# Kernel tuning notes

Hardware: AMD Instinct MI355X
Metric: run time of the kernel (lower is better)

The kernel has to match this reference:

```python
import jax, jax.numpy as jnp
import numpy as np

B, T, D, H, O = 64, 1000, 16, 1024, 8
DT, TAU, G, PROB_CONN = 0.1, 1.0, 1.5, 0.25


def setup_inputs() -> dict:
    key = jax.random.key(0)
    k_in, k_h0, k_i2h, k_mask, k_val, k_h2o = jax.random.split(key, 6)
    inp = jax.random.normal(k_in, (B, T, D), dtype=jnp.float32)
    hidden = jax.random.normal(k_h0, (B, H), dtype=jnp.float32)
    # i2h: 1/sqrt(D) * randn(H, D)
    W_i2h = jax.random.normal(k_i2h, (H, D), dtype=jnp.float32) / np.sqrt(D)
    # h2h: sparse Gaussian, connection prob PROB_CONN, no self-connections,
    # std = g / sqrt(prob_conn * H)
    mask = (jax.random.uniform(k_mask, (H, H)) < PROB_CONN).astype(jnp.float32)
    mask = mask * (1.0 - jnp.eye(H, dtype=jnp.float32))
    sigma = G / np.sqrt(PROB_CONN * H)
    W_h2h = jax.random.normal(k_val, (H, H), dtype=jnp.float32) * sigma * mask
    # h2o: 1/sqrt(H) * randn(O, H)
    W_h2o = jax.random.normal(k_h2o, (O, H), dtype=jnp.float32) / np.sqrt(H)
    return {"input": inp, "hidden": hidden, "W_i2h": W_i2h, "W_h2h": W_h2h, "W_h2o": W_h2o}


def reference(input, hidden, W_i2h, W_h2h, W_h2o):
    a = DT / TAU  # leak factor
    # precompute input projection for all timesteps: [B,T,H]
    x_proj = jnp.einsum('btd,hd->bth', input, W_i2h)
    xs = jnp.swapaxes(x_proj, 0, 1)  # [T,B,H]

    def step(h, x_t):
        h = (1.0 - a) * h + a * (jnp.tanh(h) @ W_h2h.T + x_t)
        out = jnp.tanh(h) @ W_h2o.T
        return h, (out, h)

    _, (outs, hs) = jax.lax.scan(step, hidden, xs)
    outputs = jnp.swapaxes(outs, 0, 1)  # [B,T,O]
    hiddens = jnp.swapaxes(hs, 0, 1)    # [B,T,H]
    return outputs, hiddens
```

## Files before the change

kernel.cpp:

```cpp
#include <hip/hip_runtime.h>
#include <hip/hip_bf16.h>

#define BB 64
#define TT 1000
#define DD 16
#define HH 1024
#define OO 8

#define NGRP 16
#define GB   4
#define SJ   64
#define NJS  16
#define NBLK 256
#define NTH  512

__global__ __launch_bounds__(NTH, 1) void rnn_coop(
    const float* __restrict__ x,
    const float* __restrict__ h0,
    const float* __restrict__ Wi2h,
    const float* Wh2h,
    float* __restrict__ out_h,
    float* TH,
    unsigned* flags)
{
    __shared__ __align__(16) float THl[8][4][GB][36];
    __shared__ float SC[2][GB][SJ][9];
    __shared__ float XS[2][GB][20];

    const int tid = threadIdx.x;
    const int w   = tid >> 6;
    const int l   = tid & 63;
    const int bid = blockIdx.x;
    const int bg  = bid & (NGRP - 1);
    const int js  = bid >> 4;

    const int j16 = l & 15;
    const int k4  = l >> 4;
    const int jbase = js * SJ + j16 * 4;
    const int kbase = w * 128 + k4 * 32;

    float4 w4[4][8];
#pragma unroll
    for (int jj = 0; jj < 4; ++jj) {
        const float* a = &Wh2h[(size_t)(jbase + jj) * HH + kbase];
        asm volatile(
            "global_load_dwordx4 %0, %8, off\n\t"
            "global_load_dwordx4 %1, %8, off offset:16\n\t"
            "global_load_dwordx4 %2, %8, off offset:32\n\t"
            "global_load_dwordx4 %3, %8, off offset:48\n\t"
            "global_load_dwordx4 %4, %8, off offset:64\n\t"
            "global_load_dwordx4 %5, %8, off offset:80\n\t"
            "global_load_dwordx4 %6, %8, off offset:96\n\t"
            "global_load_dwordx4 %7, %8, off offset:112\n\t"
            "s_waitcnt vmcnt(0)"
            : "=&v"(w4[jj][0]), "=&v"(w4[jj][1]), "=&v"(w4[jj][2]), "=&v"(w4[jj][3]),
              "=&v"(w4[jj][4]), "=&v"(w4[jj][5]), "=&v"(w4[jj][6]), "=&v"(w4[jj][7])
            : "v"(a));
    }

    const int fb = tid >> 6, fj = tid & 63;
    float h = 0.f;
    float wi[DD];
    if (tid < 256) {
        h = h0[(size_t)(bg * GB + fb) * HH + js * SJ + fj];
#pragma unroll
        for (int d = 0; d < DD; ++d) wi[d] = Wi2h[(js * SJ + fj) * DD + d];
        float th0 = tanhf(h);
        __hip_atomic_store(&TH[((size_t)(0 * NGRP + bg) * GB + fb) * HH + js * SJ + fj],
                           th0, __ATOMIC_RELAXED, __HIP_MEMORY_SCOPE_AGENT);
        asm volatile("s_waitcnt vmcnt(0)" ::: "memory");
        if (l == 0)
            __hip_atomic_store(&flags[((size_t)(0 * NGRP + bg) * NJS + js) * 16 + fb],
                               1u, __ATOMIC_RELAXED, __HIP_MEMORY_SCOPE_AGENT);
    }

    for (int t = 0; t < TT; ++t) {
        const int p = t & 1;

        {
            const unsigned target = (unsigned)(t + 1);
            const unsigned* fa = flags +
                ((size_t)(p * NGRP + bg) * NJS + (2 * w + (l >> 2))) * 16 + (l & 3);
            for (;;) {
                unsigned v = target;
                if (l < 8)
                    v = __hip_atomic_load(fa, __ATOMIC_RELAXED, __HIP_MEMORY_SCOPE_AGENT);
                if (__all((int)(v >= target))) break;
                __builtin_amdgcn_s_sleep(1);
            }
        }

        {
            const int sb = l >> 4, sq = l & 15;
            const float* base = TH + ((size_t)(p * NGRP + bg) * GB + sb) * HH + w * 128;
            const float* a0 = base + sq * 4;
            const float* a1 = base + (sq + 16) * 4;
            float4 v0, v1;
            asm volatile("global_load_dwordx4 %0, %2, off sc0 sc1\n\t"
                         "global_load_dwordx4 %1, %3, off sc0 sc1\n\t"
                         "s_waitcnt vmcnt(0)"
                         : "=&v"(v0), "=&v"(v1)
                         : "v"(a0), "v"(a1)
                         : "memory");
            int k40 = sq >> 3,        kk0 = (sq & 7) ^ k40;
            int k41 = (sq + 16) >> 3, kk1 = (sq & 7) ^ k41;
            *(float4*)&THl[w][k40][sb][kk0 * 4] = v0;
            *(float4*)&THl[w][k41][sb][kk1 * 4] = v1;
        }
        if (w == 0 && l < 16) {
            int sb2 = l >> 2, dq = (l & 3) * 4;
            float4 v = *(const float4*)&x[((size_t)(bg * GB + sb2) * TT + t) * DD + dq];
            *(float4*)&XS[p][sb2][dq] = v;
        }
        asm volatile("s_waitcnt lgkmcnt(0)" ::: "memory");
        __builtin_amdgcn_sched_barrier(0);

        float acc[4][4];
#pragma unroll
        for (int jj = 0; jj < 4; ++jj)
#pragma unroll
            for (int m = 0; m < 4; ++m) acc[jj][m] = 0.f;
#pragma unroll
        for (int kq = 0; kq < 8; ++kq) {
            const int kks = (kq ^ k4) * 4;
#pragma unroll
            for (int m = 0; m < 4; ++m) {
                float4 tv = *(const float4*)&THl[w][k4][m][kks];
#pragma unroll
                for (int jj = 0; jj < 4; ++jj) {
                    acc[jj][m] += w4[jj][kq].x * tv.x;
                    acc[jj][m] += w4[jj][kq].y * tv.y;
                    acc[jj][m] += w4[jj][kq].z * tv.z;
                    acc[jj][m] += w4[jj][kq].w * tv.w;
                }
            }
        }

#pragma unroll
        for (int jj = 0; jj < 4; ++jj)
#pragma unroll
            for (int m = 0; m < 4; ++m) {
                float a = acc[jj][m];
                a += __shfl_xor(a, 16, 64);
                a += __shfl_xor(a, 32, 64);
                acc[jj][m] = a;
            }
        if (k4 == 0) {
#pragma unroll
            for (int m = 0; m < 4; ++m)
#pragma unroll
                for (int jj = 0; jj < 4; ++jj)
                    SC[p][m][j16 * 4 + jj][w] = acc[jj][m];
        }

        __syncthreads();

        if (tid < 256) {
            float z = 0.f;
#pragma unroll
            for (int ww = 0; ww < 8; ++ww) z += SC[p][fb][fj][ww];
            float xp = 0.f;
#pragma unroll
            for (int d = 0; d < DD; ++d) xp += wi[d] * XS[p][fb][d];
            h = 0.9f * h + 0.1f * (z + xp);
            float th = tanhf(h);
            __hip_atomic_store(
                &TH[((size_t)((p ^ 1) * NGRP + bg) * GB + fb) * HH + js * SJ + fj],
                th, __ATOMIC_RELAXED, __HIP_MEMORY_SCOPE_AGENT);
            asm volatile("s_waitcnt vmcnt(0)" ::: "memory");
            if (l == 0 && t + 1 < TT)
                __hip_atomic_store(
                    &flags[((size_t)((p ^ 1) * NGRP + bg) * NJS + js) * 16 + fb],
                    (unsigned)(t + 2), __ATOMIC_RELAXED, __HIP_MEMORY_SCOPE_AGENT);
            out_h[((size_t)(bg * GB + fb) * TT + t) * HH + js * SJ + fj] = h;
        }
    }
}

__global__ __launch_bounds__(256) void h2o_kernel(
    const float* __restrict__ hs, const float* __restrict__ Wh2o,
    float* __restrict__ out_o)
{
    __shared__ float Wl[OO * HH];
    for (int i = threadIdx.x; i < OO * HH; i += 256) Wl[i] = Wh2o[i];
    __syncthreads();

    const int w = threadIdx.x >> 6, l = threadIdx.x & 63;
    const size_t nrows = (size_t)BB * TT;
    for (size_t row = (size_t)blockIdx.x * 4 + w; row < nrows; row += (size_t)gridDim.x * 4) {
        const float* hr = hs + row * HH;
        float po[OO] = {0.f};
#pragma unroll
        for (int i = 0; i < 16; ++i) {
            int j = l + 64 * i;
            float th = tanhf(hr[j]);
#pragma unroll
            for (int o = 0; o < OO; ++o) po[o] += th * Wl[o * HH + j];
        }
#pragma unroll
        for (int s = 32; s; s >>= 1)
#pragma unroll
            for (int o = 0; o < OO; ++o) po[o] += __shfl_down(po[o], s, 64);
        if (l == 0) {
#pragma unroll
            for (int o = 0; o < OO; ++o) out_o[row * OO + o] = po[o];
        }
    }
}

__global__ __launch_bounds__(512) void rnn_fallback(
    const float* __restrict__ x, const float* __restrict__ h0,
    const float* __restrict__ Wi2h, const float* __restrict__ W,
    const float* __restrict__ Wh2o, float* __restrict__ out_o,
    float* __restrict__ out_h)
{
    const int b = blockIdx.x, t0 = threadIdx.x, j0 = 2 * t0;
    const int wave = t0 >> 6, lane = t0 & 63;
    __shared__ float th[HH];
    __shared__ float xs[DD];
    __shared__ float ored[8][OO];
    float wi[2][DD];
#pragma unroll
    for (int d = 0; d < DD; ++d) {
        wi[0][d] = Wi2h[j0 * DD + d];
        wi[1][d] = Wi2h[(j0 + 1) * DD + d];
    }
    float wo[2][OO];
#pragma unroll
    for (int o = 0; o < OO; ++o) {
        wo[0][o] = Wh2o[o * HH + j0];
        wo[1][o] = Wh2o[o * HH + j0 + 1];
    }
    float h[2] = { h0[b * HH + j0], h0[b * HH + j0 + 1] };
    th[j0] = tanhf(h[0]); th[j0 + 1] = tanhf(h[1]);
    if (t0 < DD) xs[t0] = x[(size_t)(b * TT) * DD + t0];
    __syncthreads();
    for (int t = 0; t < TT; ++t) {
        float a0 = 0.f, a1 = 0.f;
        const float* r0 = W + (size_t)j0 * HH;
        const float* r1 = W + (size_t)(j0 + 1) * HH;
#pragma unroll 4
        for (int k = 0; k < HH; k += 4) {
            float4 t4 = *(const float4*)&th[k];
            float4 wA = *(const float4*)(r0 + k);
            float4 wB = *(const float4*)(r1 + k);
            a0 += t4.x * wA.x + t4.y * wA.y + t4.z * wA.z + t4.w * wA.w;
            a1 += t4.x * wB.x + t4.y * wB.y + t4.z * wB.z + t4.w * wB.w;
        }
        float xp0 = 0.f, xp1 = 0.f;
#pragma unroll
        for (int d = 0; d < DD; ++d) { xp0 += xs[d] * wi[0][d]; xp1 += xs[d] * wi[1][d]; }
        h[0] = 0.9f * h[0] + 0.1f * (a0 + xp0);
        h[1] = 0.9f * h[1] + 0.1f * (a1 + xp1);
        float th0 = tanhf(h[0]), th1 = tanhf(h[1]);
        *(float2*)&out_h[((size_t)b * TT + t) * HH + j0] = make_float2(h[0], h[1]);
        float po[OO];
#pragma unroll
        for (int o = 0; o < OO; ++o) po[o] = th0 * wo[0][o] + th1 * wo[1][o];
#pragma unroll
        for (int s = 32; s; s >>= 1)
#pragma unroll
            for (int o = 0; o < OO; ++o) po[o] += __shfl_down(po[o], s, 64);
        __syncthreads();
        if (lane == 0)
#pragma unroll
            for (int o = 0; o < OO; ++o) ored[wave][o] = po[o];
        th[j0] = th0; th[j0 + 1] = th1;
        if (t0 < DD && t + 1 < TT) xs[t0] = x[(size_t)(b * TT + t + 1) * DD + t0];
        __syncthreads();
        if (t0 < OO) {
            float s = 0.f;
#pragma unroll
            for (int ww = 0; ww < 8; ++ww) s += ored[ww][t0];
            out_o[((size_t)b * TT + t) * OO + t0] = s;
        }
    }
}

extern "C" void kernel_launch(void* const* d_in, const int* in_sizes, int n_in,
                              void* d_out, int out_size, void* d_ws, size_t ws_size,
                              hipStream_t stream) {
    const float* x    = (const float*)d_in[0];
    const float* h0   = (const float*)d_in[1];
    const float* Wi2h = (const float*)d_in[2];
    const float* Wh2h = (const float*)d_in[3];
    const float* Wh2o = (const float*)d_in[4];

    float* out_o = (float*)d_out;
    float* out_h = out_o + (size_t)BB * TT * OO;

    const size_t th_bytes   = (size_t)2 * NGRP * GB * HH * sizeof(float);
    const size_t flag_bytes = (size_t)2 * NGRP * NJS * 16 * sizeof(unsigned);

    if (ws_size >= th_bytes + flag_bytes) {
        float*    TH  = (float*)d_ws;
        unsigned* flg = (unsigned*)((char*)d_ws + th_bytes);
        hipMemsetAsync(flg, 0, flag_bytes, stream);
        rnn_coop<<<NBLK, NTH, 0, stream>>>(x, h0, Wi2h, Wh2h, out_h, TH, flg);
        h2o_kernel<<<2048, 256, 0, stream>>>(out_h, Wh2o, out_o);
    } else {
        rnn_fallback<<<BB, 512, 0, stream>>>(x, h0, Wi2h, Wh2h, Wh2o, out_o, out_h);
    }
}
```

Baseline: 5.007 ms.

## Split recurrent work into 512 blocks of 32 columns and precompute input projection

Adds a rnn_sj32 kernel that partitions each batch group's hidden columns into 32-wide slices, so 512 blocks of 512 threads each hold half as many h2h weights in registers. Its launch bounds allow several blocks per CU, which spreads the per-step matvec and reduction over more CUs. Separately, a new xproj_kernel precomputes the input projection for all timesteps into workspace, so each step loads one value instead of doing a 16-term dot product. In exchange, each step's barrier now involves twice as many producer blocks, and the spin-wait polls twice as many flags. The old 256-block kernel is kept as a fallback, and the path taken depends on workspace size and the occupancy query.

```diff
diff --git a/kernel.cpp b/kernel.cpp
--- a/kernel.cpp
+++ b/kernel.cpp
@@ -9,23 +9,53 @@
 
 #define NGRP 16
 #define GB   4
-#define SJ   64
-#define NJS  16
-#define NBLK 256
 #define NTH  512
 
-__global__ __launch_bounds__(NTH, 1) void rnn_coop(
+typedef unsigned long long u64;
+
+__global__ __launch_bounds__(256) void xproj_kernel(
+    const float* __restrict__ x,
+    const float* __restrict__ Wi2h,
+    float* __restrict__ xp)
+{
+    __shared__ float Wl[1024 * 17];
+    for (int i = threadIdx.x; i < 1024 * 16; i += 256)
+        Wl[(i >> 4) * 17 + (i & 15)] = Wi2h[i];
+    __syncthreads();
+
+    const int nrows = BB * TT;
+    for (int row = blockIdx.x; row < nrows; row += gridDim.x) {
+        float4 xa = *(const float4*)&x[(size_t)row * 16];
+        float4 xb = *(const float4*)&x[(size_t)row * 16 + 4];
+        float4 xc = *(const float4*)&x[(size_t)row * 16 + 8];
+        float4 xd = *(const float4*)&x[(size_t)row * 16 + 12];
+#pragma unroll
+        for (int c = 0; c < 4; ++c) {
+            int hh = threadIdx.x + 256 * c;
+            const float* wr = &Wl[hh * 17];
+            float s = xa.x * wr[0]  + xa.y * wr[1]  + xa.z * wr[2]  + xa.w * wr[3]
+                    + xb.x * wr[4]  + xb.y * wr[5]  + xb.z * wr[6]  + xb.w * wr[7]
+                    + xc.x * wr[8]  + xc.y * wr[9]  + xc.z * wr[10] + xc.w * wr[11]
+                    + xd.x * wr[12] + xd.y * wr[13] + xd.z * wr[14] + xd.w * wr[15];
+            xp[(size_t)row * HH + hh] = s;
+        }
+    }
+}
+
+template <int XPRE>
+__global__ __launch_bounds__(NTH, 4) void rnn_sj32(
     const float* __restrict__ x,
     const float* __restrict__ h0,
     const float* __restrict__ Wi2h,
     const float* Wh2h,
+    const float* __restrict__ xp,
     float* __restrict__ out_h,
     float* TH,
     unsigned* flags)
 {
-    __shared__ __align__(16) float THl[8][4][GB][36];
-    __shared__ float SC[2][GB][SJ][9];
-    __shared__ float XS[2][GB][20];
+    __shared__ __align__(16) float THl[8][4][164];
+    __shared__ float SC[2][4][32][9];
+    __shared__ float XS[2][4][20];
 
     const int tid = threadIdx.x;
     const int w   = tid >> 6;
@@ -34,9 +64,170 @@
     const int bg  = bid & (NGRP - 1);
     const int js  = bid >> 4;
 
+    const int j8 = l & 7;
+    const int k8 = l >> 3;
+    const int jbase = js * 32 + j8 * 4;
+    const int kbase = w * 128 + k8 * 16;
+
+    float4 w4[4][4];
+#pragma unroll
+    for (int jj = 0; jj < 4; ++jj) {
+        const float* a = &Wh2h[(size_t)(jbase + jj) * HH + kbase];
+        asm volatile(
+            "global_load_dwordx4 %0, %4, off\n\t"
+            "global_load_dwordx4 %1, %4, off offset:16\n\t"
+            "global_load_dwordx4 %2, %4, off offset:32\n\t"
+            "global_load_dwordx4 %3, %4, off offset:48\n\t"
+            "s_waitcnt vmcnt(0)"
+            : "=&v"(w4[jj][0]), "=&v"(w4[jj][1]), "=&v"(w4[jj][2]), "=&v"(w4[jj][3])
+            : "v"(a));
+    }
+
+    const int fj = tid & 31, fb = (tid >> 5) & 3;
+    float h = 0.f;
+    float wi[DD];
+    if (tid < 128) {
+        h = h0[(size_t)(bg * GB + fb) * HH + js * 32 + fj];
+        if (!XPRE) {
+#pragma unroll
+            for (int d = 0; d < DD; ++d) wi[d] = Wi2h[(js * 32 + fj) * DD + d];
+        }
+        float th0 = tanhf(h);
+        __hip_atomic_store(&TH[((size_t)(0 * NGRP + bg) * GB + fb) * HH + js * 32 + fj],
+                           th0, __ATOMIC_RELAXED, __HIP_MEMORY_SCOPE_AGENT);
+        asm volatile("s_waitcnt vmcnt(0)" ::: "memory");
+        if ((tid & 63) == 0)
+            __hip_atomic_store(
+                &flags[((size_t)(0 * NGRP + bg) * 32 + js) * 16 + (tid >> 6)],
+                1u, __ATOMIC_RELAXED, __HIP_MEMORY_SCOPE_AGENT);
+    }
+
+    for (int t = 0; t < TT; ++t) {
+        const int p = t & 1;
+
+        float xpv = 0.f;
+        if (XPRE && tid < 128)
+            xpv = xp[((size_t)(bg * GB + fb) * TT + t) * HH + js * 32 + fj];
+
+        {
+            const unsigned target = (unsigned)(t + 1);
+            const unsigned* fa = flags +
+                ((size_t)(p * NGRP + bg) * 32 + (4 * w + (l >> 1))) * 16 + (l & 1);
+            for (;;) {
+                unsigned v = target;
+                if (l < 8)
+                    v = __hip_atomic_load(fa, __ATOMIC_RELAXED, __HIP_MEMORY_SCOPE_AGENT);
+                if (__all((int)(v >= target))) break;
+                __builtin_amdgcn_s_sleep(1);
+            }
+        }
+
+        {
+            const int b = l & 3, Q0 = l >> 2;
+            const float* base = TH + ((size_t)(p * NGRP + bg) * GB + b) * HH + w * 128;
+            const float* a0 = base + Q0 * 4;
+            const float* a1 = base + (Q0 + 16) * 4;
+            float4 v0, v1;
+            asm volatile("global_load_dwordx4 %0, %2, off sc0 sc1\n\t"
+                         "global_load_dwordx4 %1, %3, off sc0 sc1\n\t"
+                         "s_waitcnt vmcnt(0)"
+                         : "=&v"(v0), "=&v"(v1)
+                         : "v"(a0), "v"(a1)
+                         : "memory");
+            *(float4*)&THl[w][b][(Q0 >> 2) * 20 + (Q0 & 3) * 4] = v0;
+            *(float4*)&THl[w][b][((Q0 + 16) >> 2) * 20 + (Q0 & 3) * 4] = v1;
+        }
+        if (!XPRE && w == 0 && l < 16) {
+            int sb2 = l >> 2, dq = (l & 3) * 4;
+            float4 v = *(const float4*)&x[((size_t)(bg * GB + sb2) * TT + t) * DD + dq];
+            *(float4*)&XS[p][sb2][dq] = v;
+        }
+        asm volatile("s_waitcnt lgkmcnt(0)" ::: "memory");
+        __builtin_amdgcn_sched_barrier(0);
+
+        float acc[4][4];
+#pragma unroll
+        for (int jj = 0; jj < 4; ++jj)
+#pragma unroll
+            for (int m = 0; m < 4; ++m) acc[jj][m] = 0.f;
+#pragma unroll
+        for (int kq = 0; kq < 4; ++kq) {
+#pragma unroll
+            for (int m = 0; m < 4; ++m) {
+                float4 tv = *(const float4*)&THl[w][m][k8 * 20 + kq * 4];
+#pragma unroll
+                for (int jj = 0; jj < 4; ++jj) {
+                    acc[jj][m] += w4[jj][kq].x * tv.x;
+                    acc[jj][m] += w4[jj][kq].y * tv.y;
+                    acc[jj][m] += w4[jj][kq].z * tv.z;
+                    acc[jj][m] += w4[jj][kq].w * tv.w;
+                }
+            }
+        }
+
+#pragma unroll
+        for (int jj = 0; jj < 4; ++jj)
+#pragma unroll
+            for (int m = 0; m < 4; ++m) {
+                float a = acc[jj][m];
+                a += __shfl_xor(a, 8, 64);
+                a += __shfl_xor(a, 16, 64);
+                a += __shfl_xor(a, 32, 64);
+                acc[jj][m] = a;
+            }
+        if (l < 8) {
+#pragma unroll
+            for (int m = 0; m < 4; ++m)
+#pragma unroll
+                for (int jj = 0; jj < 4; ++jj)
+                    SC[p][m][l * 4 + jj][w] = acc[jj][m];
+        }
+
+        __syncthreads();
+
+        if (tid < 128) {
+            float z = 0.f;
+#pragma unroll
+            for (int ww = 0; ww < 8; ++ww) z += SC[p][fb][fj][ww];
+            if (!XPRE) {
+                xpv = 0.f;
+#pragma unroll
+                for (int d = 0; d < DD; ++d) xpv += wi[d] * XS[p][fb][d];
+            }
+            h = 0.9f * h + 0.1f * (z + xpv);
+            float th = tanhf(h);
+            __hip_atomic_store(
+                &TH[((size_t)((p ^ 1) * NGRP + bg) * GB + fb) * HH + js * 32 + fj],
+                th, __ATOMIC_RELAXED, __HIP_MEMORY_SCOPE_AGENT);
+            asm volatile("s_waitcnt vmcnt(0)" ::: "memory");
+            if ((tid & 63) == 0 && t + 1 < TT)
+                __hip_atomic_store(
+                    &flags[((size_t)((p ^ 1) * NGRP + bg) * 32 + js) * 16 + (tid >> 6)],
+                    (unsigned)(t + 2), __ATOMIC_RELAXED, __HIP_MEMORY_SCOPE_AGENT);
+            out_h[((size_t)(bg * GB + fb) * TT + t) * HH + js * 32 + fj] = h;
+        }
+    }
+}
+
+__global__ __launch_bounds__(NTH, 1) void rnn_coop_t2(
+    const float* __restrict__ x, const float* __restrict__ h0,
+    const float* __restrict__ Wi2h, const float* Wh2h,
+    float* __restrict__ out_h, float* TH, unsigned* flags)
+{
+    __shared__ __align__(16) float THl[8][4][GB][36];
+    __shared__ float SC[2][GB][64][9];
+    __shared__ float XS[2][GB][20];
+
+    const int tid = threadIdx.x;
+    const int w   = tid >> 6;
+    const int l   = tid & 63;
+    const int bid = blockIdx.x;
+    const int bg  = bid & (NGRP - 1);
+    const int js  = bid >> 4;
+
     const int j16 = l & 15;
     const int k4  = l >> 4;
-    const int jbase = js * SJ + j16 * 4;
+    const int jbase = js * 64 + j16 * 4;
     const int kbase = w * 128 + k4 * 32;
 
     float4 w4[4][8];
@@ -62,25 +253,24 @@
     float h = 0.f;
     float wi[DD];
     if (tid < 256) {
-        h = h0[(size_t)(bg * GB + fb) * HH + js * SJ + fj];
-#pragma unroll
-        for (int d = 0; d < DD; ++d) wi[d] = Wi2h[(js * SJ + fj) * DD + d];
+        h = h0[(size_t)(bg * GB + fb) * HH + js * 64 + fj];
+#pragma unroll
+        for (int d = 0; d < DD; ++d) wi[d] = Wi2h[(js * 64 + fj) * DD + d];
         float th0 = tanhf(h);
-        __hip_atomic_store(&TH[((size_t)(0 * NGRP + bg) * GB + fb) * HH + js * SJ + fj],
+        __hip_atomic_store(&TH[((size_t)(0 * NGRP + bg) * GB + fb) * HH + js * 64 + fj],
                            th0, __ATOMIC_RELAXED, __HIP_MEMORY_SCOPE_AGENT);
         asm volatile("s_waitcnt vmcnt(0)" ::: "memory");
         if (l == 0)
-            __hip_atomic_store(&flags[((size_t)(0 * NGRP + bg) * NJS + js) * 16 + fb],
+            __hip_atomic_store(&flags[((size_t)(0 * NGRP + bg) * 16 + js) * 16 + fb],
                                1u, __ATOMIC_RELAXED, __HIP_MEMORY_SCOPE_AGENT);
     }
 
     for (int t = 0; t < TT; ++t) {
         const int p = t & 1;
-
         {
             const unsigned target = (unsigned)(t + 1);
             const unsigned* fa = flags +
-                ((size_t)(p * NGRP + bg) * NJS + (2 * w + (l >> 2))) * 16 + (l & 3);
+                ((size_t)(p * NGRP + bg) * 16 + (2 * w + (l >> 2))) * 16 + (l & 3);
             for (;;) {
                 unsigned v = target;
                 if (l < 8)
@@ -89,7 +279,6 @@
                 __builtin_amdgcn_s_sleep(1);
             }
         }
-
         {
             const int sb = l >> 4, sq = l & 15;
             const float* base = TH + ((size_t)(p * NGRP + bg) * GB + sb) * HH + w * 128;
@@ -135,7 +324,6 @@
                 }
             }
         }
-
 #pragma unroll
         for (int jj = 0; jj < 4; ++jj)
 #pragma unroll
@@ -152,27 +340,25 @@
                 for (int jj = 0; jj < 4; ++jj)
                     SC[p][m][j16 * 4 + jj][w] = acc[jj][m];
         }
-
         __syncthreads();
-
         if (tid < 256) {
             float z = 0.f;
 #pragma unroll
             for (int ww = 0; ww < 8; ++ww) z += SC[p][fb][fj][ww];
-            float xp = 0.f;
-#pragma unroll
-            for (int d = 0; d < DD; ++d) xp += wi[d] * XS[p][fb][d];
-            h = 0.9f * h + 0.1f * (z + xp);
+            float xpv = 0.f;
+#pragma unroll
+            for (int d = 0; d < DD; ++d) xpv += wi[d] * XS[p][fb][d];
+            h = 0.9f * h + 0.1f * (z + xpv);
             float th = tanhf(h);
             __hip_atomic_store(
-                &TH[((size_t)((p ^ 1) * NGRP + bg) * GB + fb) * HH + js * SJ + fj],
+                &TH[((size_t)((p ^ 1) * NGRP + bg) * GB + fb) * HH + js * 64 + fj],
                 th, __ATOMIC_RELAXED, __HIP_MEMORY_SCOPE_AGENT);
             asm volatile("s_waitcnt vmcnt(0)" ::: "memory");
             if (l == 0 && t + 1 < TT)
                 __hip_atomic_store(
-                    &flags[((size_t)((p ^ 1) * NGRP + bg) * NJS + js) * 16 + fb],
+                    &flags[((size_t)((p ^ 1) * NGRP + bg) * 16 + js) * 16 + fb],
                     (unsigned)(t + 2), __ATOMIC_RELAXED, __HIP_MEMORY_SCOPE_AGENT);
-            out_h[((size_t)(bg * GB + fb) * TT + t) * HH + js * SJ + fj] = h;
+            out_h[((size_t)(bg * GB + fb) * TT + t) * HH + js * 64 + fj] = h;
         }
     }
 }
@@ -289,14 +475,37 @@
     float* out_o = (float*)d_out;
     float* out_h = out_o + (size_t)BB * TT * OO;
 
-    const size_t th_bytes   = (size_t)2 * NGRP * GB * HH * sizeof(float);
-    const size_t flag_bytes = (size_t)2 * NGRP * NJS * 16 * sizeof(unsigned);
-
-    if (ws_size >= th_bytes + flag_bytes) {
+    const size_t XP_BYTES   = (size_t)BB * TT * HH * sizeof(float);
+    const size_t TH_BYTES   = (size_t)2 * NGRP * GB * HH * sizeof(float);
+    const size_t FLG1_BYTES = (size_t)2 * NGRP * 32 * 16 * sizeof(unsigned);
+    const size_t FLG2_BYTES = (size_t)2 * NGRP * 16 * 16 * sizeof(unsigned);
+
+    int occ1 = 0, occ0 = 0;
+    (void)hipOccupancyMaxActiveBlocksPerMultiprocessor(
+        &occ1, reinterpret_cast<const void*>(&rnn_sj32<1>), NTH, 0);
+    (void)hipOccupancyMaxActiveBlocksPerMultiprocessor(
+        &occ0, reinterpret_cast<const void*>(&rnn_sj32<0>), NTH, 0);
+
+    if (ws_size >= XP_BYTES + TH_BYTES + FLG1_BYTES && occ1 >= 2) {
+        float*    xp  = (float*)d_ws;
+        float*    TH  = (float*)((char*)d_ws + XP_BYTES);
+        unsigned* flg = (unsigned*)((char*)d_ws + XP_BYTES + TH_BYTES);
+        hipMemsetAsync(flg, 0, FLG1_BYTES, stream);
+        xproj_kernel<<<512, 256, 0, stream>>>(x, Wi2h, xp);
+        rnn_sj32<1><<<512, NTH, 0, stream>>>(x, h0, Wi2h, Wh2h, xp, out_h, TH, flg);
+        h2o_kernel<<<2048, 256, 0, stream>>>(out_h, Wh2o, out_o);
+    } else if (ws_size >= TH_BYTES + FLG1_BYTES && occ0 >= 2) {
         float*    TH  = (float*)d_ws;
-        unsigned* flg = (unsigned*)((char*)d_ws + th_bytes);
-        hipMemsetAsync(flg, 0, flag_bytes, stream);
-        rnn_coop<<<NBLK, NTH, 0, stream>>>(x, h0, Wi2h, Wh2h, out_h, TH, flg);
+        unsigned* flg = (unsigned*)((char*)d_ws + TH_BYTES);
+        hipMemsetAsync(flg, 0, FLG1_BYTES, stream);
+        rnn_sj32<0><<<512, NTH, 0, stream>>>(x, h0, Wi2h, Wh2h, (const float*)d_ws,
+                                             out_h, TH, flg);
+        h2o_kernel<<<2048, 256, 0, stream>>>(out_h, Wh2o, out_o);
+    } else if (ws_size >= TH_BYTES + FLG2_BYTES) {
+        float*    TH  = (float*)d_ws;
+        unsigned* flg = (unsigned*)((char*)d_ws + TH_BYTES);
+        hipMemsetAsync(flg, 0, FLG2_BYTES, stream);
+        rnn_coop_t2<<<256, NTH, 0, stream>>>(x, h0, Wi2h, Wh2h, out_h, TH, flg);
         h2o_kernel<<<2048, 256, 0, stream>>>(out_h, Wh2o, out_o);
     } else {
         rnn_fallback<<<BB, 512, 0, stream>>>(x, h0, Wi2h, Wh2h, Wh2o, out_o, out_h);
```

Result: no change. 4.995 ms (-0.2%).
